# Optimization experiments

Measured on AMD Instinct MI355X. Metric: run time of the kernel, lower is better.

The kernel has to match this reference:

```python
import jax, jax.numpy as jnp
import numpy as np

B, L, E, H = 4, 4096, 1024, 16
HD = E // H
I = 4096  # intermediate_size = 4*E
RMS_EPS = 1e-6
ATTN_EPS = 1e-6
GATE_INIT = 0.1  # 0.1 + 0.05*layer_idx, layer_idx=0


def rmsnorm(x, w, eps=RMS_EPS):
    xf = x.astype(jnp.float32)
    var = jnp.mean(xf * xf, axis=-1, keepdims=True)
    return w * (xf * jax.lax.rsqrt(var + eps)).astype(x.dtype)


def rotate_half(x):
    d = x.shape[-1] // 2
    return jnp.concatenate([-x[..., d:], x[..., :d]], axis=-1)


def setup_inputs() -> dict:
    key = jax.random.key(0)
    ks = jax.random.split(key, 16)
    h = jax.random.normal(ks[0], (B, L, E), jnp.float32)
    c = jax.random.normal(ks[1], (B, E), jnp.float32)
    # standard RoPE tables, shape (L, HD)
    pos = jnp.arange(L, dtype=jnp.float32)
    inv = 1.0 / (10000.0 ** (jnp.arange(0, HD, 2, dtype=jnp.float32) / HD))
    fr = pos[:, None] * inv[None, :]
    emb = jnp.concatenate([fr, fr], axis=-1)
    cos, sin = jnp.cos(emb), jnp.sin(emb)
    s = 0.02
    Wq = jax.random.normal(ks[2], (E, E), jnp.float32) * s
    Wk = jax.random.normal(ks[3], (E, E), jnp.float32) * s
    Wv = jax.random.normal(ks[4], (E, E), jnp.float32) * s
    Wo = jax.random.normal(ks[5], (E, E), jnp.float32) * s
    Wg = jax.random.normal(ks[6], (I, E), jnp.float32) * s
    Wu = jax.random.normal(ks[7], (I, E), jnp.float32) * s
    Wd = jax.random.normal(ks[8], (E, I), jnp.float32) * s
    w_norm1 = jnp.ones((E,), jnp.float32)
    w_norm2 = jnp.ones((E,), jnp.float32)
    Wada = jax.random.normal(ks[9], (6 * E, E), jnp.float32) * 0.01
    bada = np.zeros((6 * E,), np.float32)
    bada[2 * E:3 * E] = GATE_INIT  # gate_msa
    bada[5 * E:6 * E] = GATE_INIT  # gate_mlp
    bada = jnp.asarray(bada)
    return {"h": h, "c": c, "cos": cos, "sin": sin, "Wq": Wq, "Wk": Wk,
            "Wv": Wv, "Wo": Wo, "Wg": Wg, "Wu": Wu, "Wd": Wd,
            "w_norm1": w_norm1, "w_norm2": w_norm2, "Wada": Wada, "bada": bada}


def reference(h, c, cos, sin, Wq, Wk, Wv, Wo, Wg, Wu, Wd, w_norm1, w_norm2, Wada, bada):
    # adaLN modulation: (B, 6E) -> six (B,1,E) chunks
    mod = c @ Wada.T + bada
    sh1, sc1, g1, sh2, sc2, g2 = [m[:, None, :] for m in jnp.split(mod, 6, axis=-1)]

    # --- attention branch ---
    x = rmsnorm(h, w_norm1) * (1.0 + sc1) + sh1  # modulate
    q = jax.nn.silu(x @ Wq.T).reshape(B, L, H, HD).transpose(0, 2, 1, 3)  # (B,H,L,hd)
    k = jax.nn.silu(x @ Wk.T).reshape(B, L, H, HD).transpose(0, 2, 1, 3)
    v = (x @ Wv.T).reshape(B, L, H, HD).transpose(0, 2, 1, 3)
    cs = cos[None, None]  # (1,1,L,hd)
    sn = sin[None, None]
    q = q * cs + rotate_half(q) * sn
    k = k * cs + rotate_half(k) * sn
    # cosFormer sin/cos feature map; m = max(src,tgt) = L
    idx = (np.pi / 2) * jnp.arange(1, L + 1, dtype=jnp.float32) / L  # (L,)
    sw = jnp.sin(idx)[None, None, :, None]
    cw = jnp.cos(idx)[None, None, :, None]
    q_ = jnp.concatenate([q * sw, q * cw], axis=-1)  # (B,H,L,2hd)
    k_ = jnp.concatenate([k * sw, k * cw], axis=-1)
    # non-causal linear attention: K^T V first (O(L))
    kv = jnp.einsum('bhld,bhlm->bhdm', k_, v)             # (B,H,2hd,hd)
    z = 1.0 / jnp.maximum(jnp.einsum('bhld,bhd->bhl', q_, k_.sum(axis=2)), ATTN_EPS)
    attn = jnp.einsum('bhld,bhdm,bhl->bhlm', q_, kv, z)   # (B,H,L,hd)
    attn = attn.transpose(0, 2, 1, 3).reshape(B, L, E) @ Wo.T
    h = h + g1 * attn  # bias_dropout_add_scale, eval mode

    # --- MLP branch ---
    x = rmsnorm(h, w_norm2) * (1.0 + sc2) + sh2
    mlp = (jax.nn.silu(x @ Wg.T) * (x @ Wu.T)) @ Wd.T
    return h + g2 * mlp
```

## Files before the change

kernel.cpp:

```cpp
#include <hip/hip_runtime.h>
#include <hip/hip_bf16.h>

#define BB 4
#define LL 4096
#define EE 1024
#define HH 16
#define II 4096
#define MM (BB*LL)

using f32x4 = __attribute__((ext_vector_type(4))) float;
using s16x8 = __attribute__((ext_vector_type(8))) short;
using u32x4 = __attribute__((ext_vector_type(4))) unsigned int;

__device__ __forceinline__ unsigned short f2bf(float f) {
  union { float f; unsigned u; } x; x.f = f;
  unsigned r = x.u + 0x7fffu + ((x.u >> 16) & 1u);
  return (unsigned short)(r >> 16);
}
__device__ __forceinline__ float bf2f(unsigned short s) {
  union { unsigned u; float f; } x; x.u = ((unsigned)s) << 16;
  return x.f;
}
__device__ __forceinline__ unsigned packbf(float lo, float hi) {
  return ((unsigned)f2bf(hi) << 16) | (unsigned)f2bf(lo);
}
__device__ __forceinline__ float silu_f(float x) { return x / (1.0f + expf(-x)); }

__global__ __launch_bounds__(256) void k_mod(const float* __restrict__ c,
    const float* __restrict__ Wada, const float* __restrict__ bada,
    float* __restrict__ mod) {
  __shared__ float cs[EE];
  int b = blockIdx.y;
  int n = blockIdx.x * 256 + threadIdx.x;
  for (int i = threadIdx.x; i < EE; i += 256) cs[i] = c[b*EE + i];
  __syncthreads();
  const float4* wp = (const float4*)(Wada + (size_t)n * EE);
  float acc = 0.f;
  for (int k = 0; k < EE/4; k++) {
    float4 t = wp[k];
    acc += t.x*cs[4*k] + t.y*cs[4*k+1] + t.z*cs[4*k+2] + t.w*cs[4*k+3];
  }
  mod[(size_t)b*6*EE + n] = acc + bada[n];
}

__global__ __launch_bounds__(256) void k_coef(const float* __restrict__ mod,
    const float* __restrict__ w1, const float* __restrict__ w2,
    float* __restrict__ cf1, float* __restrict__ cf2) {
  int k = blockIdx.x * 256 + threadIdx.x;
  int b = blockIdx.y;
  const float* mb = mod + (size_t)b*6*EE;
  cf1[(size_t)b*2048 + k]        = w1[k] * (1.0f + mb[EE + k]);
  cf1[(size_t)b*2048 + 1024 + k] = mb[k];
  cf2[(size_t)b*2048 + k]        = w2[k] * (1.0f + mb[4*EE + k]);
  cf2[(size_t)b*2048 + 1024 + k] = mb[3*EE + k];
}

__global__ __launch_bounds__(256) void k_rsig(const float* __restrict__ in,
    float* __restrict__ rsig) {
  int row = blockIdx.x;
  int t = threadIdx.x;
  float4 v = ((const float4*)(in + (size_t)row * EE))[t];
  float ss = v.x*v.x + v.y*v.y + v.z*v.z + v.w*v.w;
  #pragma unroll
  for (int o = 32; o > 0; o >>= 1) ss += __shfl_down(ss, o, 64);
  __shared__ float red[4];
  if ((t & 63) == 0) red[t >> 6] = ss;
  __syncthreads();
  float tot = red[0] + red[1] + red[2] + red[3];
  if (t == 0) rsig[row] = 1.0f / sqrtf(tot * (1.0f/1024.0f) + 1e-6f);
}

__global__ __launch_bounds__(256) void k_f2b(const float* __restrict__ s,
    unsigned short* __restrict__ d, int n4) {
  int i = blockIdx.x * 256 + threadIdx.x;
  if (i >= n4) return;
  float4 v = ((const float4*)s)[i];
  ushort4 u; u.x = f2bf(v.x); u.y = f2bf(v.y); u.z = f2bf(v.z); u.w = f2bf(v.w);
  ((ushort4*)d)[i] = u;
}

__global__ __launch_bounds__(256) void k_sgemm_qk(
    const float* __restrict__ Ah, const float* __restrict__ W,
    const float* __restrict__ rsig, const float* __restrict__ cf,
    const float* __restrict__ cosT, const float* __restrict__ sinT,
    float* __restrict__ outq) {
  __shared__ float As[8][128];
  __shared__ float Bs[8][128];
  __shared__ float c1s[1024];
  __shared__ float c0s[1024];
  int t = threadIdx.x;
  int tx = t & 15, ty = t >> 4;
  int bm = blockIdx.x, bn = blockIdx.y;
  int srow = t >> 1, sk = (t & 1) * 4;
  int bidx = bm >> 5;
  for (int i = t; i < 1024; i += 256) {
    c1s[i] = cf[(size_t)bidx*2048 + i];
    c0s[i] = cf[(size_t)bidx*2048 + 1024 + i];
  }
  int arow = bm*128 + srow;
  float rsA = rsig[arow];
  const float* ap = Ah + (size_t)arow*EE + sk;
  const float* bp = W + (size_t)(bn*128 + srow)*EE + sk;
  float acc[8][8];
  #pragma unroll
  for (int i = 0; i < 8; i++)
    #pragma unroll
    for (int j = 0; j < 8; j++) acc[i][j] = 0.f;
  float4 pa = *(const float4*)ap;
  float4 pb = *(const float4*)bp;
  int c0 = (tx < 8) ? tx*4 : 64 + (tx - 8)*4;
  __syncthreads();
  for (int k0 = 0; k0 < EE; k0 += 8) {
    int kb = k0 + sk;
    As[sk+0][srow] = fmaf(pa.x*rsA, c1s[kb+0], c0s[kb+0]);
    As[sk+1][srow] = fmaf(pa.y*rsA, c1s[kb+1], c0s[kb+1]);
    As[sk+2][srow] = fmaf(pa.z*rsA, c1s[kb+2], c0s[kb+2]);
    As[sk+3][srow] = fmaf(pa.w*rsA, c1s[kb+3], c0s[kb+3]);
    Bs[sk+0][srow] = pb.x; Bs[sk+1][srow] = pb.y; Bs[sk+2][srow] = pb.z; Bs[sk+3][srow] = pb.w;
    __syncthreads();
    if (k0 + 8 < EE) {
      pa = *(const float4*)(ap + k0 + 8);
      pb = *(const float4*)(bp + k0 + 8);
    }
    #pragma unroll
    for (int k = 0; k < 8; k++) {
      float4 a0 = *(const float4*)&As[k][ty*8];
      float4 a1 = *(const float4*)&As[k][ty*8+4];
      float4 b0 = *(const float4*)&Bs[k][c0];
      float4 b1 = *(const float4*)&Bs[k][c0+32];
      float av[8] = {a0.x,a0.y,a0.z,a0.w,a1.x,a1.y,a1.z,a1.w};
      float bv[8] = {b0.x,b0.y,b0.z,b0.w,b1.x,b1.y,b1.z,b1.w};
      #pragma unroll
      for (int i = 0; i < 8; i++)
        #pragma unroll
        for (int j = 0; j < 8; j++)
          acc[i][j] = fmaf(av[i], bv[j], acc[i][j]);
    }
    __syncthreads();
  }
  int head = bn*2 + (tx >= 8 ? 1 : 0);
  int d0 = (tx < 8) ? tx*4 : (tx - 8)*4;
  #pragma unroll
  for (int i = 0; i < 8; i++) {
    int m = bm*128 + ty*8 + i;
    int b = m >> 12, l = m & 4095;
    const float* cp = cosT + (size_t)l*64;
    const float* sp = sinT + (size_t)l*64;
    float4 cl  = *(const float4*)(cp + d0);
    float4 slv = *(const float4*)(sp + d0);
    float4 chv = *(const float4*)(cp + d0 + 32);
    float4 shv = *(const float4*)(sp + d0 + 32);
    float sA0 = silu_f(acc[i][0]), sA1 = silu_f(acc[i][1]), sA2 = silu_f(acc[i][2]), sA3 = silu_f(acc[i][3]);
    float sB0 = silu_f(acc[i][4]), sB1 = silu_f(acc[i][5]), sB2 = silu_f(acc[i][6]), sB3 = silu_f(acc[i][7]);
    float q00 = sA0*cl.x - sB0*slv.x;
    float q01 = sA1*cl.y - sB1*slv.y;
    float q02 = sA2*cl.z - sB2*slv.z;
    float q03 = sA3*cl.w - sB3*slv.w;
    float q10 = sB0*chv.x + sA0*shv.x;
    float q11 = sB1*chv.y + sA1*shv.y;
    float q12 = sB2*chv.z + sA2*shv.z;
    float q13 = sB3*chv.w + sA3*shv.w;
    float* op = outq + ((size_t)(b*HH + head)*LL + l)*64;
    *(float4*)(op + d0)      = make_float4(q00, q01, q02, q03);
    *(float4*)(op + d0 + 32) = make_float4(q10, q11, q12, q13);
  }
}

template<int EPI, int KD, int AMODE>
__global__ __launch_bounds__(256) void k_gemm_bt(
    const float* __restrict__ Af, const unsigned short* __restrict__ Ab,
    const unsigned short* __restrict__ Bw,
    const float* __restrict__ rsig, const float* __restrict__ cf,
    const float* __restrict__ res, const float* __restrict__ mod,
    unsigned short* __restrict__ outb, float* __restrict__ outf) {
  __shared__ unsigned short As[128][40];
  __shared__ unsigned short Bs[128][40];
  __shared__ float c1s[1024];
  __shared__ float c0s[1024];
  int t = threadIdx.x;
  int bm = blockIdx.x, bn = blockIdx.y;
  int w = t >> 6, lane = t & 63;
  int wm = (w >> 1) * 64, wn = (w & 1) * 64;
  f32x4 acc[4][4];
  #pragma unroll
  for (int i = 0; i < 4; i++)
    #pragma unroll
    for (int j = 0; j < 4; j++) acc[i][j] = (f32x4){0.f, 0.f, 0.f, 0.f};
  int srow = t >> 1, koff = (t & 1) * 16;
  int arow = bm*128 + srow;
  const unsigned short* bp = Bw + (size_t)(bn*128 + srow)*KD + koff;
  u32x4 pb0 = *(const u32x4*)bp;
  u32x4 pb1 = *(const u32x4*)(bp + 8);
  float rsA = 0.f;
  const float* apf = nullptr;
  const unsigned short* apb = nullptr;
  float4 ha0, ha1, ha2, ha3;
  u32x4 pa0, pa1;
  if constexpr (AMODE == 1) {
    int bidx = bm >> 5;
    for (int i = t; i < 1024; i += 256) {
      c1s[i] = cf[(size_t)bidx*2048 + i];
      c0s[i] = cf[(size_t)bidx*2048 + 1024 + i];
    }
    rsA = rsig[arow];
    apf = Af + (size_t)arow*KD + koff;
    ha0 = *(const float4*)apf;
    ha1 = *(const float4*)(apf + 4);
    ha2 = *(const float4*)(apf + 8);
    ha3 = *(const float4*)(apf + 12);
    __syncthreads();
  } else {
    apb = Ab + (size_t)arow*KD + koff;
    pa0 = *(const u32x4*)apb;
    pa1 = *(const u32x4*)(apb + 8);
  }
  int r16 = lane & 15, kg = lane >> 4;
  for (int k0 = 0; k0 < KD; k0 += 32) {
    if constexpr (AMODE == 1) {
      int kb = k0 + koff;
      float x0  = fmaf(ha0.x*rsA, c1s[kb+0],  c0s[kb+0]);
      float x1  = fmaf(ha0.y*rsA, c1s[kb+1],  c0s[kb+1]);
      float x2  = fmaf(ha0.z*rsA, c1s[kb+2],  c0s[kb+2]);
      float x3  = fmaf(ha0.w*rsA, c1s[kb+3],  c0s[kb+3]);
      float x4  = fmaf(ha1.x*rsA, c1s[kb+4],  c0s[kb+4]);
      float x5  = fmaf(ha1.y*rsA, c1s[kb+5],  c0s[kb+5]);
      float x6  = fmaf(ha1.z*rsA, c1s[kb+6],  c0s[kb+6]);
      float x7  = fmaf(ha1.w*rsA, c1s[kb+7],  c0s[kb+7]);
      float x8  = fmaf(ha2.x*rsA, c1s[kb+8],  c0s[kb+8]);
      float x9  = fmaf(ha2.y*rsA, c1s[kb+9],  c0s[kb+9]);
      float x10 = fmaf(ha2.z*rsA, c1s[kb+10], c0s[kb+10]);
      float x11 = fmaf(ha2.w*rsA, c1s[kb+11], c0s[kb+11]);
      float x12 = fmaf(ha3.x*rsA, c1s[kb+12], c0s[kb+12]);
      float x13 = fmaf(ha3.y*rsA, c1s[kb+13], c0s[kb+13]);
      float x14 = fmaf(ha3.z*rsA, c1s[kb+14], c0s[kb+14]);
      float x15 = fmaf(ha3.w*rsA, c1s[kb+15], c0s[kb+15]);
      u32x4 ua, ub;
      ua[0] = packbf(x0, x1);  ua[1] = packbf(x2, x3);
      ua[2] = packbf(x4, x5);  ua[3] = packbf(x6, x7);
      ub[0] = packbf(x8, x9);  ub[1] = packbf(x10, x11);
      ub[2] = packbf(x12, x13); ub[3] = packbf(x14, x15);
      *(u32x4*)&As[srow][koff]   = ua;
      *(u32x4*)&As[srow][koff+8] = ub;
    } else {
      *(u32x4*)&As[srow][koff]   = pa0;
      *(u32x4*)&As[srow][koff+8] = pa1;
    }
    *(u32x4*)&Bs[srow][koff]   = pb0;
    *(u32x4*)&Bs[srow][koff+8] = pb1;
    __syncthreads();
    if (k0 + 32 < KD) {
      if constexpr (AMODE == 1) {
        ha0 = *(const float4*)(apf + k0 + 32);
        ha1 = *(const float4*)(apf + k0 + 36);
        ha2 = *(const float4*)(apf + k0 + 40);
        ha3 = *(const float4*)(apf + k0 + 44);
      } else {
        pa0 = *(const u32x4*)(apb + k0 + 32);
        pa1 = *(const u32x4*)(apb + k0 + 40);
      }
      pb0 = *(const u32x4*)(bp + k0 + 32);
      pb1 = *(const u32x4*)(bp + k0 + 40);
    }
    s16x8 af[4], bfr[4];
    #pragma unroll
    for (int i = 0; i < 4; i++) af[i]  = *(const s16x8*)&As[wm + i*16 + r16][kg*8];
    #pragma unroll
    for (int j = 0; j < 4; j++) bfr[j] = *(const s16x8*)&Bs[wn + j*16 + r16][kg*8];
    #pragma unroll
    for (int i = 0; i < 4; i++)
      #pragma unroll
      for (int j = 0; j < 4; j++)
        acc[i][j] = __builtin_amdgcn_mfma_f32_16x16x32_bf16(af[i], bfr[j], acc[i][j], 0, 0, 0);
    __syncthreads();
  }
  #pragma unroll
  for (int i = 0; i < 4; i++) {
    #pragma unroll
    for (int j = 0; j < 4; j++) {
      int nn = bn*128 + wn + j*16 + r16;
      #pragma unroll
      for (int r = 0; r < 4; r++) {
        int mm = bm*128 + wm + i*16 + kg*4 + r;
        float v = acc[i][j][r];
        if constexpr (EPI == 0) {
          int b = mm >> 12, l = mm & 4095, hh = nn >> 6, dd = nn & 63;
          outb[(((size_t)(b*HH + hh))*LL + l)*64 + dd] = f2bf(v);
        } else if constexpr (EPI == 1) {
          int b = mm >> 12;
          size_t o = (size_t)mm*EE + nn;
          outf[o] = res[o] + mod[(size_t)b*6*EE + 2*EE + nn] * v;
        } else if constexpr (EPI == 2) {
          outb[(size_t)mm*II + nn] = f2bf(silu_f(v));
        } else if constexpr (EPI == 3) {
          size_t o = (size_t)mm*II + nn;
          outb[o] = f2bf(bf2f(outb[o]) * v);
        } else {
          int b = mm >> 12;
          size_t o = (size_t)mm*EE + nn;
          outf[o] = res[o] + mod[(size_t)b*6*EE + 5*EE + nn] * v;
        }
      }
    }
  }
}

__global__ __launch_bounds__(256) void k_kvpart(const float* __restrict__ kr,
    const unsigned short* __restrict__ vtb, float* __restrict__ kvp) {
  int bi = blockIdx.x;
  int bh = bi >> 3, ch = bi & 7;
  const float* kp = kr + ((size_t)bh*LL + ch*512)*64;
  const unsigned short* vp = vtb + ((size_t)bh*LL + ch*512)*64;
  __shared__ float k8[8][64];
  __shared__ float v8[8][64];
  __shared__ float sw8[8], cw8[8];
  int t = threadIdx.x;
  int d = t >> 2, mq = (t & 3) * 16;
  float accS[16], accC[16];
  #pragma unroll
  for (int q = 0; q < 16; q++) { accS[q] = 0.f; accC[q] = 0.f; }
  float ksS = 0.f, ksC = 0.f;
  for (int l0 = 0; l0 < 512; l0 += 8) {
    __syncthreads();
    #pragma unroll
    for (int rep = 0; rep < 2; rep++) {
      int idx = rep*256 + t;
      k8[idx>>6][idx&63] = kp[(size_t)(l0 + (idx>>6))*64 + (idx&63)];
      v8[idx>>6][idx&63] = bf2f(vp[(size_t)(l0 + (idx>>6))*64 + (idx&63)]);
    }
    if (t < 8) {
      int gl = ch*512 + l0 + t;
      float idxv = 1.5707964f * (float)(gl + 1) * (1.0f/4096.0f);
      sw8[t] = sinf(idxv);
      cw8[t] = cosf(idxv);
    }
    __syncthreads();
    #pragma unroll
    for (int l = 0; l < 8; l++) {
      float kd = k8[l][d];
      float s = kd * sw8[l];
      float c = kd * cw8[l];
      ksS += s; ksC += c;
      const float4* vv = (const float4*)&v8[l][mq];
      #pragma unroll
      for (int q = 0; q < 4; q++) {
        float4 x = vv[q];
        accS[4*q+0] = fmaf(s, x.x, accS[4*q+0]);
        accS[4*q+1] = fmaf(s, x.y, accS[4*q+1]);
        accS[4*q+2] = fmaf(s, x.z, accS[4*q+2]);
        accS[4*q+3] = fmaf(s, x.w, accS[4*q+3]);
        accC[4*q+0] = fmaf(c, x.x, accC[4*q+0]);
        accC[4*q+1] = fmaf(c, x.y, accC[4*q+1]);
        accC[4*q+2] = fmaf(c, x.z, accC[4*q+2]);
        accC[4*q+3] = fmaf(c, x.w, accC[4*q+3]);
      }
    }
  }
  float* op = kvp + (size_t)bi * 8320;
  #pragma unroll
  for (int q = 0; q < 16; q++) {
    op[d*64 + mq + q]        = accS[q];
    op[4096 + d*64 + mq + q] = accC[q];
  }
  if (mq == 0) { op[8192 + d] = ksS; op[8256 + d] = ksC; }
}

__global__ __launch_bounds__(256) void k_kvred(const float* __restrict__ kvp,
    float* __restrict__ kvb) {
  int bh = blockIdx.x;
  for (int i = threadIdx.x; i < 8320; i += 256) {
    float s = 0.f;
    #pragma unroll
    for (int c = 0; c < 8; c++) s += kvp[((size_t)bh*8 + c)*8320 + i];
    kvb[(size_t)bh*8320 + i] = s;
  }
}

__global__ __launch_bounds__(256) void k_z(const float* __restrict__ qr,
    const float* __restrict__ kvb, float* __restrict__ zb) {
  int bh = blockIdx.x >> 6, lc = blockIdx.x & 63;
  __shared__ float ksS_s[64], ksC_s[64];
  int t = threadIdx.x;
  if (t < 64) ksS_s[t] = kvb[(size_t)bh*8320 + 8192 + t];
  else if (t < 128) ksC_s[t-64] = kvb[(size_t)bh*8320 + 8256 + (t-64)];
  __syncthreads();
  int l = lc*64 + (t >> 2), part = t & 3;
  const float4* qp = (const float4*)(qr + ((size_t)bh*LL + l)*64 + part*16);
  float A = 0.f, Bv = 0.f;
  #pragma unroll
  for (int q = 0; q < 4; q++) {
    float4 x = qp[q];
    int kb = part*16 + 4*q;
    A  += x.x*ksS_s[kb] + x.y*ksS_s[kb+1] + x.z*ksS_s[kb+2] + x.w*ksS_s[kb+3];
    Bv += x.x*ksC_s[kb] + x.y*ksC_s[kb+1] + x.z*ksC_s[kb+2] + x.w*ksC_s[kb+3];
  }
  A  += __shfl_xor(A, 1, 64);  A  += __shfl_xor(A, 2, 64);
  Bv += __shfl_xor(Bv, 1, 64); Bv += __shfl_xor(Bv, 2, 64);
  if (part == 0) {
    float idxv = 1.5707964f * (float)(l + 1) * (1.0f/4096.0f);
    float denom = sinf(idxv)*A + cosf(idxv)*Bv;
    zb[(size_t)bh*LL + l] = 1.0f / fmaxf(denom, 1e-6f);
  }
}

__global__ __launch_bounds__(256) void k_attn(const float* __restrict__ qr,
    const float* __restrict__ kvb, const float* __restrict__ zb,
    unsigned short* __restrict__ attnb) {
  int bh = blockIdx.x >> 4, lc = blockIdx.x & 15;
  int t = threadIdx.x, w = t >> 6, lane = t & 63;
  const float* kvp_ = kvb + (size_t)bh*8320;
  float kvS[64], kvC[64];
  #pragma unroll
  for (int d = 0; d < 64; d++) kvS[d] = kvp_[d*64 + lane];
  #pragma unroll
  for (int d = 0; d < 64; d++) kvC[d] = kvp_[4096 + d*64 + lane];
  int b = bh >> 4, hh = bh & 15;
  int lbase = lc*256 + w*64;
  for (int li = 0; li < 64; li++) {
    int l = lbase + li;
    const float* qp = qr + ((size_t)bh*LL + l)*64;
    float qv = qp[lane];
    float z = zb[(size_t)bh*LL + l];
    float a0 = 0.f, a1 = 0.f, a2 = 0.f, a3 = 0.f;
    float b0 = 0.f, b1 = 0.f, b2 = 0.f, b3 = 0.f;
    #pragma unroll
    for (int d = 0; d < 64; d += 4) {
      float q0 = __uint_as_float(__builtin_amdgcn_readlane(__float_as_uint(qv), d+0));
      float q1 = __uint_as_float(__builtin_amdgcn_readlane(__float_as_uint(qv), d+1));
      float q2 = __uint_as_float(__builtin_amdgcn_readlane(__float_as_uint(qv), d+2));
      float q3 = __uint_as_float(__builtin_amdgcn_readlane(__float_as_uint(qv), d+3));
      a0 = fmaf(q0, kvS[d+0], a0);
      a1 = fmaf(q1, kvS[d+1], a1);
      a2 = fmaf(q2, kvS[d+2], a2);
      a3 = fmaf(q3, kvS[d+3], a3);
      b0 = fmaf(q0, kvC[d+0], b0);
      b1 = fmaf(q1, kvC[d+1], b1);
      b2 = fmaf(q2, kvC[d+2], b2);
      b3 = fmaf(q3, kvC[d+3], b3);
    }
    float A = (a0 + a1) + (a2 + a3);
    float Bv = (b0 + b1) + (b2 + b3);
    float idxv = 1.5707964f * (float)(l + 1) * (1.0f/4096.0f);
    float num = sinf(idxv)*A + cosf(idxv)*Bv;
    attnb[(((size_t)b*LL + l)*HH + hh)*64 + lane] = f2bf(num * z);
  }
}

extern "C" void kernel_launch(void* const* d_in, const int* in_sizes, int n_in,
                              void* d_out, int out_size, void* d_ws, size_t ws_size,
                              hipStream_t stream) {
  const float* h    = (const float*)d_in[0];
  const float* c    = (const float*)d_in[1];
  const float* cosT = (const float*)d_in[2];
  const float* sinT = (const float*)d_in[3];
  const float* Wq   = (const float*)d_in[4];
  const float* Wk   = (const float*)d_in[5];
  const float* Wv   = (const float*)d_in[6];
  const float* Wo   = (const float*)d_in[7];
  const float* Wg   = (const float*)d_in[8];
  const float* Wu   = (const float*)d_in[9];
  const float* Wd   = (const float*)d_in[10];
  const float* w1   = (const float*)d_in[11];
  const float* w2   = (const float*)d_in[12];
  const float* Wada = (const float*)d_in[13];
  const float* bada = (const float*)d_in[14];
  float* out = (float*)d_out;

  constexpr size_t BIG_SZ   = (size_t)MM * II * 2;
  constexpr size_t WS_NEEDED = BIG_SZ + 131072 + 32768*2 + 65536*2
      + 1048576 + 2129920 + 2097152*2 + 8388608*3;
  if (ws_size < WS_NEEDED) return;

  char* p = (char*)d_ws;
  char* big = p;                               p += BIG_SZ;
  float* mod = (float*)p;                      p += 131072;
  float* cf1 = (float*)p;                      p += 32768;
  float* cf2 = (float*)p;                      p += 32768;
  float* rsig1 = (float*)p;                    p += 65536;
  float* rsig2 = (float*)p;                    p += 65536;
  float* zb  = (float*)p;                      p += 1048576;
  float* kvb = (float*)p;                      p += 2129920;
  unsigned short* Wvb = (unsigned short*)p;    p += 2097152;
  unsigned short* Wob = (unsigned short*)p;    p += 2097152;
  unsigned short* Wgb = (unsigned short*)p;    p += 8388608;
  unsigned short* Wub = (unsigned short*)p;    p += 8388608;
  unsigned short* Wdb = (unsigned short*)p;    p += 8388608;
  float* kr            = (float*)big;
  unsigned short* vtb  = (unsigned short*)(big + 67108864);
  float* kvp           = (float*)(big + 100663296);
  float* qr            = (float*)big;
  unsigned short* attnb= (unsigned short*)(big + 67108864);
  unsigned short* Gb   = (unsigned short*)big;

  k_mod<<<dim3(24, BB), 256, 0, stream>>>(c, Wada, bada, mod);
  k_coef<<<dim3(4, BB), 256, 0, stream>>>(mod, w1, w2, cf1, cf2);
  k_rsig<<<MM, 256, 0, stream>>>(h, rsig1);
  k_f2b<<<1024, 256, 0, stream>>>(Wv, Wvb, EE*EE/4);
  k_f2b<<<1024, 256, 0, stream>>>(Wo, Wob, EE*EE/4);
  k_f2b<<<4096, 256, 0, stream>>>(Wg, Wgb, II*EE/4);
  k_f2b<<<4096, 256, 0, stream>>>(Wu, Wub, II*EE/4);
  k_f2b<<<4096, 256, 0, stream>>>(Wd, Wdb, EE*II/4);

  k_sgemm_qk<<<dim3(128, 8), 256, 0, stream>>>(h, Wk, rsig1, cf1, cosT, sinT, kr);
  k_gemm_bt<0, EE, 1><<<dim3(128, 8), 256, 0, stream>>>(
      h, nullptr, Wvb, rsig1, cf1, nullptr, nullptr, vtb, nullptr);
  k_kvpart<<<BB*HH*8, 256, 0, stream>>>(kr, vtb, kvp);
  k_kvred<<<BB*HH, 256, 0, stream>>>(kvp, kvb);

  k_sgemm_qk<<<dim3(128, 8), 256, 0, stream>>>(h, Wq, rsig1, cf1, cosT, sinT, qr);
  k_z<<<BB*HH*(LL/64), 256, 0, stream>>>(qr, kvb, zb);
  k_attn<<<BB*HH*(LL/256), 256, 0, stream>>>(qr, kvb, zb, attnb);

  k_gemm_bt<1, EE, 0><<<dim3(128, 8), 256, 0, stream>>>(
      nullptr, attnb, Wob, nullptr, nullptr, h, mod, nullptr, out);

  k_rsig<<<MM, 256, 0, stream>>>(out, rsig2);
  k_gemm_bt<2, EE, 1><<<dim3(128, 32), 256, 0, stream>>>(
      out, nullptr, Wgb, rsig2, cf2, nullptr, nullptr, Gb, nullptr);
  k_gemm_bt<3, EE, 1><<<dim3(128, 32), 256, 0, stream>>>(
      out, nullptr, Wub, rsig2, cf2, nullptr, nullptr, Gb, nullptr);
  k_gemm_bt<4, II, 0><<<dim3(128, 8), 256, 0, stream>>>(
      nullptr, Gb, Wdb, nullptr, nullptr, out, mod, nullptr, out);
}
```

Measured before the change: 2.148 ms.

## Use split-bf16 MFMA for Q projection, async LDS loads, and near-zero denominator fixup

Several changes land together. The normalized activations are precomputed once into hi/lo bf16 pairs. The fp32 SIMT Q GEMM is replaced by a three-term split-bf16 MFMA GEMM, which emulates near-fp32 accuracy on matrix cores. All bf16 GEMMs now stage tiles with global_load_lds direct-to-LDS copies and an XOR swizzle instead of register staging. To guard accuracy, rows whose attention denominator is near zero are collected with an atomic list and recomputed in double precision. This adds a pre-pass kernel, extra MFMAs, and a fixup kernel whose cost depends on how many rows are flagged.

```diff
diff --git a/kernel.cpp b/kernel.cpp
--- a/kernel.cpp
+++ b/kernel.cpp
@@ -25,6 +25,12 @@
   return ((unsigned)f2bf(hi) << 16) | (unsigned)f2bf(lo);
 }
 __device__ __forceinline__ float silu_f(float x) { return x / (1.0f + expf(-x)); }
+
+__device__ __forceinline__ void gll16(const void* g, void* l) {
+  __builtin_amdgcn_global_load_lds(
+      (const __attribute__((address_space(1))) unsigned int*)g,
+      (__attribute__((address_space(3))) unsigned int*)l, 16, 0, 0);
+}
 
 __global__ __launch_bounds__(256) void k_mod(const float* __restrict__ c,
     const float* __restrict__ Wada, const float* __restrict__ bada,
@@ -79,7 +85,31 @@
   ((ushort4*)d)[i] = u;
 }
 
-__global__ __launch_bounds__(256) void k_sgemm_qk(
+__global__ __launch_bounds__(256) void k_split1(const float* __restrict__ h,
+    const float* __restrict__ rsig, const float* __restrict__ cf,
+    unsigned short* __restrict__ xh, unsigned short* __restrict__ xl) {
+  int row = blockIdx.x;
+  int t = threadIdx.x;
+  int b = row >> 12;
+  float rs = rsig[row];
+  const float* cfb = cf + (size_t)b*2048;
+  float4 v  = ((const float4*)(h + (size_t)row*EE))[t];
+  float4 c1 = ((const float4*)cfb)[t];
+  float4 c0 = ((const float4*)(cfb + 1024))[t];
+  float x0 = fmaf(v.x*rs, c1.x, c0.x);
+  float x1 = fmaf(v.y*rs, c1.y, c0.y);
+  float x2 = fmaf(v.z*rs, c1.z, c0.z);
+  float x3 = fmaf(v.w*rs, c1.w, c0.w);
+  ushort4 uh, ul;
+  uh.x = f2bf(x0); ul.x = f2bf(x0 - bf2f(uh.x));
+  uh.y = f2bf(x1); ul.y = f2bf(x1 - bf2f(uh.y));
+  uh.z = f2bf(x2); ul.z = f2bf(x2 - bf2f(uh.z));
+  uh.w = f2bf(x3); ul.w = f2bf(x3 - bf2f(uh.w));
+  ((ushort4*)(xh + (size_t)row*EE))[t] = uh;
+  ((ushort4*)(xl + (size_t)row*EE))[t] = ul;
+}
+
+__global__ __launch_bounds__(256) void k_sgemmK(
     const float* __restrict__ Ah, const float* __restrict__ W,
     const float* __restrict__ rsig, const float* __restrict__ cf,
     const float* __restrict__ cosT, const float* __restrict__ sinT,
@@ -129,7 +159,7 @@
       float4 b0 = *(const float4*)&Bs[k][c0];
       float4 b1 = *(const float4*)&Bs[k][c0+32];
       float av[8] = {a0.x,a0.y,a0.z,a0.w,a1.x,a1.y,a1.z,a1.w};
-      float bv[8] = {b0.x,b0.y,b0.z,b0.w,b1.x,b1.y,b1.z,b1.w};
+      float bv[8]  = {b0.x,b0.y,b0.z,b0.w,b1.x,b1.y,b1.z,b1.w};
       #pragma unroll
       for (int i = 0; i < 8; i++)
         #pragma unroll
@@ -166,57 +196,162 @@
   }
 }
 
+__global__ __launch_bounds__(256) void k_qk(
+    const unsigned short* __restrict__ xh, const unsigned short* __restrict__ xl,
+    const float* __restrict__ W,
+    const float* __restrict__ cosT, const float* __restrict__ sinT,
+    float* __restrict__ outq) {
+  __shared__ unsigned short Ah[128*32];
+  __shared__ unsigned short Al[128*32];
+  __shared__ unsigned short Bh[64*40];
+  __shared__ unsigned short Bl[64*40];
+  int t = threadIdx.x, w = t >> 6, lane = t & 63;
+  int bm = blockIdx.x, bn = blockIdx.y;
+  int wm = (w & 1) * 64;
+  int wn = (w >> 1) * 16;
+  int r16 = lane & 15, kg = lane >> 4;
+  int rin = lane >> 2, slot = lane & 3;
+  int ar0 = w*32 + rin, ar1 = ar0 + 16;
+  const unsigned short* ahg0 = xh + (size_t)(bm*128 + ar0)*EE + (size_t)((((ar0>>1)&3) ^ slot) * 8);
+  const unsigned short* ahg1 = xh + (size_t)(bm*128 + ar1)*EE + (size_t)((((ar1>>1)&3) ^ slot) * 8);
+  const unsigned short* alg0 = xl + (size_t)(bm*128 + ar0)*EE + (size_t)((((ar0>>1)&3) ^ slot) * 8);
+  const unsigned short* alg1 = xl + (size_t)(bm*128 + ar1)*EE + (size_t)((((ar1>>1)&3) ^ slot) * 8);
+  unsigned short* ahl0 = &Ah[(w*32 + 0) * 32];
+  unsigned short* ahl1 = &Ah[(w*32 + 16) * 32];
+  unsigned short* all0 = &Al[(w*32 + 0) * 32];
+  unsigned short* all1 = &Al[(w*32 + 16) * 32];
+  int srow = t >> 2, koff = (t & 3) * 8;
+  const float* bp = W + (size_t)(bn*64 + srow)*EE + koff;
+  float4 pb0 = *(const float4*)(bp + 0);
+  float4 pb1 = *(const float4*)(bp + 4);
+  f32x4 acc[4][2];
+  #pragma unroll
+  for (int i = 0; i < 4; i++) { acc[i][0] = (f32x4){0,0,0,0}; acc[i][1] = (f32x4){0,0,0,0}; }
+
+  for (int k0 = 0; k0 < EE; k0 += 32) {
+    gll16(ahg0 + k0, ahl0);
+    gll16(ahg1 + k0, ahl1);
+    gll16(alg0 + k0, all0);
+    gll16(alg1 + k0, all1);
+    {
+      unsigned short h0 = f2bf(pb0.x), h1 = f2bf(pb0.y), h2 = f2bf(pb0.z), h3 = f2bf(pb0.w);
+      unsigned short h4 = f2bf(pb1.x), h5 = f2bf(pb1.y), h6 = f2bf(pb1.z), h7 = f2bf(pb1.w);
+      unsigned short l0 = f2bf(pb0.x - bf2f(h0)), l1 = f2bf(pb0.y - bf2f(h1));
+      unsigned short l2 = f2bf(pb0.z - bf2f(h2)), l3 = f2bf(pb0.w - bf2f(h3));
+      unsigned short l4 = f2bf(pb1.x - bf2f(h4)), l5 = f2bf(pb1.y - bf2f(h5));
+      unsigned short l6 = f2bf(pb1.z - bf2f(h6)), l7 = f2bf(pb1.w - bf2f(h7));
+      u32x4 uh, ul;
+      uh[0] = ((unsigned)h1<<16)|h0; uh[1] = ((unsigned)h3<<16)|h2;
+      uh[2] = ((unsigned)h5<<16)|h4; uh[3] = ((unsigned)h7<<16)|h6;
+      ul[0] = ((unsigned)l1<<16)|l0; ul[1] = ((unsigned)l3<<16)|l2;
+      ul[2] = ((unsigned)l5<<16)|l4; ul[3] = ((unsigned)l7<<16)|l6;
+      *(u32x4*)&Bh[srow*40 + koff] = uh;
+      *(u32x4*)&Bl[srow*40 + koff] = ul;
+    }
+    __syncthreads();
+    if (k0 + 32 < EE) {
+      pb0 = *(const float4*)(bp + k0 + 32);
+      pb1 = *(const float4*)(bp + k0 + 36);
+    }
+    int brow0 = wn + r16, brow1 = wn + 32 + r16;
+    s16x8 bh0 = *(const s16x8*)&Bh[brow0*40 + kg*8];
+    s16x8 bl0 = *(const s16x8*)&Bl[brow0*40 + kg*8];
+    s16x8 bh1 = *(const s16x8*)&Bh[brow1*40 + kg*8];
+    s16x8 bl1 = *(const s16x8*)&Bl[brow1*40 + kg*8];
+    #pragma unroll
+    for (int i = 0; i < 4; i++) {
+      int row = wm + i*16 + r16;
+      int sw = ((((row>>1)&3) ^ kg) << 3);
+      s16x8 ah = *(const s16x8*)&Ah[row*32 + sw];
+      s16x8 al = *(const s16x8*)&Al[row*32 + sw];
+      acc[i][0] = __builtin_amdgcn_mfma_f32_16x16x32_bf16(ah, bh0, acc[i][0], 0, 0, 0);
+      acc[i][0] = __builtin_amdgcn_mfma_f32_16x16x32_bf16(ah, bl0, acc[i][0], 0, 0, 0);
+      acc[i][0] = __builtin_amdgcn_mfma_f32_16x16x32_bf16(al, bh0, acc[i][0], 0, 0, 0);
+      acc[i][1] = __builtin_amdgcn_mfma_f32_16x16x32_bf16(ah, bh1, acc[i][1], 0, 0, 0);
+      acc[i][1] = __builtin_amdgcn_mfma_f32_16x16x32_bf16(ah, bl1, acc[i][1], 0, 0, 0);
+      acc[i][1] = __builtin_amdgcn_mfma_f32_16x16x32_bf16(al, bh1, acc[i][1], 0, 0, 0);
+    }
+    __syncthreads();
+  }
+  int d = wn + r16;
+  #pragma unroll
+  for (int i = 0; i < 4; i++) {
+    #pragma unroll
+    for (int r = 0; r < 4; r++) {
+      int mm = bm*128 + wm + i*16 + kg*4 + r;
+      int b = mm >> 12, l = mm & 4095;
+      const float* cp = cosT + (size_t)l*64;
+      const float* sp = sinT + (size_t)l*64;
+      float sl = silu_f(acc[i][0][r]);
+      float sh = silu_f(acc[i][1][r]);
+      float qlo = sl*cp[d]      - sh*sp[d];
+      float qhi = sh*cp[d + 32] + sl*sp[d + 32];
+      float* op = outq + (((size_t)(b*HH + bn))*LL + l)*64;
+      op[d]      = qlo;
+      op[d + 32] = qhi;
+    }
+  }
+}
+
 template<int EPI, int KD, int AMODE>
-__global__ __launch_bounds__(256) void k_gemm_bt(
+__global__ __launch_bounds__(256) void k_gemm2(
     const float* __restrict__ Af, const unsigned short* __restrict__ Ab,
     const unsigned short* __restrict__ Bw,
     const float* __restrict__ rsig, const float* __restrict__ cf,
     const float* __restrict__ res, const float* __restrict__ mod,
     unsigned short* __restrict__ outb, float* __restrict__ outf) {
-  __shared__ unsigned short As[128][40];
-  __shared__ unsigned short Bs[128][40];
-  __shared__ float c1s[1024];
-  __shared__ float c0s[1024];
-  int t = threadIdx.x;
+  constexpr int APAD = (AMODE == 1) ? 40 : 32;
+  __shared__ unsigned short As[128 * APAD];
+  __shared__ unsigned short Bs[128 * 32];
+  __shared__ float c1s[(AMODE == 1) ? 1024 : 1];
+  __shared__ float c0s[(AMODE == 1) ? 1024 : 1];
+  int t = threadIdx.x, w = t >> 6, lane = t & 63;
   int bm = blockIdx.x, bn = blockIdx.y;
-  int w = t >> 6, lane = t & 63;
   int wm = (w >> 1) * 64, wn = (w & 1) * 64;
-  f32x4 acc[4][4];
-  #pragma unroll
-  for (int i = 0; i < 4; i++)
-    #pragma unroll
-    for (int j = 0; j < 4; j++) acc[i][j] = (f32x4){0.f, 0.f, 0.f, 0.f};
+  int rin = lane >> 2, slot = lane & 3;
+  int brow0 = w*32 + rin, brow1 = brow0 + 16;
+  const unsigned short* bg0 = Bw + (size_t)(bn*128 + brow0)*KD + (size_t)((((brow0>>1)&3) ^ slot) * 8);
+  const unsigned short* bg1 = Bw + (size_t)(bn*128 + brow1)*KD + (size_t)((((brow1>>1)&3) ^ slot) * 8);
+  unsigned short* bl0 = &Bs[(w*32 + 0) * 32];
+  unsigned short* bl1 = &Bs[(w*32 + 16) * 32];
+  const unsigned short* ag0 = nullptr; const unsigned short* ag1 = nullptr;
+  unsigned short* al0 = nullptr; unsigned short* al1 = nullptr;
+  const float* apf = nullptr;
+  float rsA = 0.f;
   int srow = t >> 1, koff = (t & 1) * 16;
-  int arow = bm*128 + srow;
-  const unsigned short* bp = Bw + (size_t)(bn*128 + srow)*KD + koff;
-  u32x4 pb0 = *(const u32x4*)bp;
-  u32x4 pb1 = *(const u32x4*)(bp + 8);
-  float rsA = 0.f;
-  const float* apf = nullptr;
-  const unsigned short* apb = nullptr;
   float4 ha0, ha1, ha2, ha3;
-  u32x4 pa0, pa1;
   if constexpr (AMODE == 1) {
     int bidx = bm >> 5;
     for (int i = t; i < 1024; i += 256) {
       c1s[i] = cf[(size_t)bidx*2048 + i];
       c0s[i] = cf[(size_t)bidx*2048 + 1024 + i];
     }
-    rsA = rsig[arow];
-    apf = Af + (size_t)arow*KD + koff;
-    ha0 = *(const float4*)apf;
+    rsA = rsig[bm*128 + srow];
+    apf = Af + (size_t)(bm*128 + srow)*KD + koff;
+    ha0 = *(const float4*)(apf + 0);
     ha1 = *(const float4*)(apf + 4);
     ha2 = *(const float4*)(apf + 8);
     ha3 = *(const float4*)(apf + 12);
     __syncthreads();
   } else {
-    apb = Ab + (size_t)arow*KD + koff;
-    pa0 = *(const u32x4*)apb;
-    pa1 = *(const u32x4*)(apb + 8);
-  }
+    ag0 = Ab + (size_t)(bm*128 + brow0)*KD + (size_t)((((brow0>>1)&3) ^ slot) * 8);
+    ag1 = Ab + (size_t)(bm*128 + brow1)*KD + (size_t)((((brow1>>1)&3) ^ slot) * 8);
+    al0 = &As[(w*32 + 0) * 32];
+    al1 = &As[(w*32 + 16) * 32];
+  }
+  f32x4 acc[4][4];
+  #pragma unroll
+  for (int i = 0; i < 4; i++)
+    #pragma unroll
+    for (int j = 0; j < 4; j++) acc[i][j] = (f32x4){0.f, 0.f, 0.f, 0.f};
   int r16 = lane & 15, kg = lane >> 4;
   for (int k0 = 0; k0 < KD; k0 += 32) {
-    if constexpr (AMODE == 1) {
+    gll16(bg0 + k0, bl0);
+    gll16(bg1 + k0, bl1);
+    if constexpr (AMODE == 0) {
+      gll16(ag0 + k0, al0);
+      gll16(ag1 + k0, al1);
+    } else {
       int kb = k0 + koff;
       float x0  = fmaf(ha0.x*rsA, c1s[kb+0],  c0s[kb+0]);
       float x1  = fmaf(ha0.y*rsA, c1s[kb+1],  c0s[kb+1]);
@@ -235,37 +370,36 @@
       float x14 = fmaf(ha3.z*rsA, c1s[kb+14], c0s[kb+14]);
       float x15 = fmaf(ha3.w*rsA, c1s[kb+15], c0s[kb+15]);
       u32x4 ua, ub;
-      ua[0] = packbf(x0, x1);  ua[1] = packbf(x2, x3);
-      ua[2] = packbf(x4, x5);  ua[3] = packbf(x6, x7);
-      ub[0] = packbf(x8, x9);  ub[1] = packbf(x10, x11);
+      ua[0] = packbf(x0, x1);   ua[1] = packbf(x2, x3);
+      ua[2] = packbf(x4, x5);   ua[3] = packbf(x6, x7);
+      ub[0] = packbf(x8, x9);   ub[1] = packbf(x10, x11);
       ub[2] = packbf(x12, x13); ub[3] = packbf(x14, x15);
-      *(u32x4*)&As[srow][koff]   = ua;
-      *(u32x4*)&As[srow][koff+8] = ub;
-    } else {
-      *(u32x4*)&As[srow][koff]   = pa0;
-      *(u32x4*)&As[srow][koff+8] = pa1;
-    }
-    *(u32x4*)&Bs[srow][koff]   = pb0;
-    *(u32x4*)&Bs[srow][koff+8] = pb1;
-    __syncthreads();
-    if (k0 + 32 < KD) {
-      if constexpr (AMODE == 1) {
+      *(u32x4*)&As[srow*APAD + koff]     = ua;
+      *(u32x4*)&As[srow*APAD + koff + 8] = ub;
+    }
+    __syncthreads();
+    if constexpr (AMODE == 1) {
+      if (k0 + 32 < KD) {
         ha0 = *(const float4*)(apf + k0 + 32);
         ha1 = *(const float4*)(apf + k0 + 36);
         ha2 = *(const float4*)(apf + k0 + 40);
         ha3 = *(const float4*)(apf + k0 + 44);
-      } else {
-        pa0 = *(const u32x4*)(apb + k0 + 32);
-        pa1 = *(const u32x4*)(apb + k0 + 40);
       }
-      pb0 = *(const u32x4*)(bp + k0 + 32);
-      pb1 = *(const u32x4*)(bp + k0 + 40);
     }
     s16x8 af[4], bfr[4];
     #pragma unroll
-    for (int i = 0; i < 4; i++) af[i]  = *(const s16x8*)&As[wm + i*16 + r16][kg*8];
-    #pragma unroll
-    for (int j = 0; j < 4; j++) bfr[j] = *(const s16x8*)&Bs[wn + j*16 + r16][kg*8];
+    for (int i = 0; i < 4; i++) {
+      int row = wm + i*16 + r16;
+      if constexpr (AMODE == 0)
+        af[i] = *(const s16x8*)&As[row*32 + ((((row>>1)&3) ^ kg) << 3)];
+      else
+        af[i] = *(const s16x8*)&As[row*APAD + (kg << 3)];
+    }
+    #pragma unroll
+    for (int j = 0; j < 4; j++) {
+      int row = wn + j*16 + r16;
+      bfr[j] = *(const s16x8*)&Bs[row*32 + ((((row>>1)&3) ^ kg) << 3)];
+    }
     #pragma unroll
     for (int i = 0; i < 4; i++)
       #pragma unroll
@@ -375,8 +509,11 @@
   }
 }
 
+__global__ void k_zero(int* __restrict__ cnt) { if (threadIdx.x == 0) *cnt = 0; }
+
 __global__ __launch_bounds__(256) void k_z(const float* __restrict__ qr,
-    const float* __restrict__ kvb, float* __restrict__ zb) {
+    const float* __restrict__ kvb, float* __restrict__ zb,
+    int* __restrict__ list, int* __restrict__ cnt) {
   int bh = blockIdx.x >> 6, lc = blockIdx.x & 63;
   __shared__ float ksS_s[64], ksC_s[64];
   int t = threadIdx.x;
@@ -398,7 +535,67 @@
   if (part == 0) {
     float idxv = 1.5707964f * (float)(l + 1) * (1.0f/4096.0f);
     float denom = sinf(idxv)*A + cosf(idxv)*Bv;
-    zb[(size_t)bh*LL + l] = 1.0f / fmaxf(denom, 1e-6f);
+    int gid = bh*LL + l;
+    zb[gid] = 1.0f / fmaxf(denom, 1e-6f);
+    if (fabsf(denom) < 0.05f) {
+      int idx = atomicAdd(cnt, 1);
+      list[idx] = gid;
+    }
+  }
+}
+
+__global__ __launch_bounds__(256) void k_zfix(const float* __restrict__ h,
+    const float* __restrict__ rsig, const float* __restrict__ cf,
+    const float* __restrict__ Wq,
+    const float* __restrict__ cosT, const float* __restrict__ sinT,
+    const float* __restrict__ kvb, const int* __restrict__ list,
+    const int* __restrict__ cnt, float* __restrict__ zb) {
+  __shared__ float xs[1024];
+  __shared__ double qd[64];
+  __shared__ double sq[64];
+  int n = *cnt;
+  int t = threadIdx.x;
+  for (int i = blockIdx.x; i < n; i += gridDim.x) {
+    int gid = list[i];
+    int bh = gid >> 12, l = gid & 4095;
+    int b = bh >> 4, hh = bh & 15;
+    int row = b*4096 + l;
+    float rs = rsig[row];
+    const float* cfb = cf + (size_t)b*2048;
+    for (int k = t; k < 1024; k += 256)
+      xs[k] = fmaf(h[(size_t)row*1024 + k]*rs, cfb[k], cfb[1024 + k]);
+    __syncthreads();
+    int j = t >> 2, s = t & 3;
+    const float* wrow = Wq + (size_t)(hh*64 + j)*1024 + s*256;
+    double acc = 0.0;
+    for (int k = 0; k < 256; k++)
+      acc += (double)wrow[k] * (double)xs[s*256 + k];
+    acc += __shfl_xor(acc, 1, 64);
+    acc += __shfl_xor(acc, 2, 64);
+    if (s == 0) qd[j] = acc;
+    __syncthreads();
+    if (t < 64) {
+      double qv = qd[t];
+      sq[t] = qv / (1.0 + exp(-qv));
+    }
+    __syncthreads();
+    if (t == 0) {
+      const float* cp = cosT + (size_t)l*64;
+      const float* sp = sinT + (size_t)l*64;
+      const float* ksS = kvb + (size_t)bh*8320 + 8192;
+      const float* ksC = kvb + (size_t)bh*8320 + 8256;
+      double dS = 0.0, dC = 0.0;
+      for (int d = 0; d < 64; d++) {
+        double rot = (d < 32) ? -sq[d + 32] : sq[d - 32];
+        double qe = sq[d]*(double)cp[d] + rot*(double)sp[d];
+        dS += qe * (double)ksS[d];
+        dC += qe * (double)ksC[d];
+      }
+      double idxv = 1.5707963267948966 * (double)(l + 1) / 4096.0;
+      float denom = (float)(sin(idxv)*dS + cos(idxv)*dC);
+      zb[gid] = 1.0f / fmaxf(denom, 1e-6f);
+    }
+    __syncthreads();
   }
 }
 
@@ -484,12 +681,16 @@
   unsigned short* Wgb = (unsigned short*)p;    p += 8388608;
   unsigned short* Wub = (unsigned short*)p;    p += 8388608;
   unsigned short* Wdb = (unsigned short*)p;    p += 8388608;
-  float* kr            = (float*)big;
+  unsigned short* xh   = (unsigned short*)big;
+  unsigned short* xl   = (unsigned short*)(big + 33554432);
   unsigned short* vtb  = (unsigned short*)(big + 67108864);
   float* kvp           = (float*)(big + 100663296);
-  float* qr            = (float*)big;
-  unsigned short* attnb= (unsigned short*)(big + 67108864);
+  float* qr            = (float*)(big + 67108864);
+  int* zf_cnt          = (int*)big;
+  int* zf_list         = (int*)(big + 256);
+  unsigned short* attnb= (unsigned short*)big;
   unsigned short* Gb   = (unsigned short*)big;
+  float* kr            = (float*)d_out;
 
   k_mod<<<dim3(24, BB), 256, 0, stream>>>(c, Wada, bada, mod);
   k_coef<<<dim3(4, BB), 256, 0, stream>>>(mod, w1, w2, cf1, cf2);
@@ -499,25 +700,29 @@
   k_f2b<<<4096, 256, 0, stream>>>(Wg, Wgb, II*EE/4);
   k_f2b<<<4096, 256, 0, stream>>>(Wu, Wub, II*EE/4);
   k_f2b<<<4096, 256, 0, stream>>>(Wd, Wdb, EE*II/4);
-
-  k_sgemm_qk<<<dim3(128, 8), 256, 0, stream>>>(h, Wk, rsig1, cf1, cosT, sinT, kr);
-  k_gemm_bt<0, EE, 1><<<dim3(128, 8), 256, 0, stream>>>(
-      h, nullptr, Wvb, rsig1, cf1, nullptr, nullptr, vtb, nullptr);
+  k_split1<<<MM, 256, 0, stream>>>(h, rsig1, cf1, xh, xl);
+
+  k_sgemmK<<<dim3(128, 8), 256, 0, stream>>>(h, Wk, rsig1, cf1, cosT, sinT, kr);
+  k_gemm2<0, EE, 0><<<dim3(128, 8), 256, 0, stream>>>(
+      nullptr, xh, Wvb, nullptr, nullptr, nullptr, nullptr, vtb, nullptr);
   k_kvpart<<<BB*HH*8, 256, 0, stream>>>(kr, vtb, kvp);
   k_kvred<<<BB*HH, 256, 0, stream>>>(kvp, kvb);
 
-  k_sgemm_qk<<<dim3(128, 8), 256, 0, stream>>>(h, Wq, rsig1, cf1, cosT, sinT, qr);
-  k_z<<<BB*HH*(LL/64), 256, 0, stream>>>(qr, kvb, zb);
+  k_qk<<<dim3(128, 16), 256, 0, stream>>>(xh, xl, Wq, cosT, sinT, qr);
+  k_zero<<<1, 64, 0, stream>>>(zf_cnt);
+  k_z<<<BB*HH*(LL/64), 256, 0, stream>>>(qr, kvb, zb, zf_list, zf_cnt);
+  k_zfix<<<120, 256, 0, stream>>>(h, rsig1, cf1, Wq, cosT, sinT, kvb,
+                                  zf_list, zf_cnt, zb);
   k_attn<<<BB*HH*(LL/256), 256, 0, stream>>>(qr, kvb, zb, attnb);
 
-  k_gemm_bt<1, EE, 0><<<dim3(128, 8), 256, 0, stream>>>(
+  k_gemm2<1, EE, 0><<<dim3(128, 8), 256, 0, stream>>>(
       nullptr, attnb, Wob, nullptr, nullptr, h, mod, nullptr, out);
 
   k_rsig<<<MM, 256, 0, stream>>>(out, rsig2);
-  k_gemm_bt<2, EE, 1><<<dim3(128, 32), 256, 0, stream>>>(
+  k_gemm2<2, EE, 1><<<dim3(128, 32), 256, 0, stream>>>(
       out, nullptr, Wgb, rsig2, cf2, nullptr, nullptr, Gb, nullptr);
-  k_gemm_bt<3, EE, 1><<<dim3(128, 32), 256, 0, stream>>>(
+  k_gemm2<3, EE, 1><<<dim3(128, 32), 256, 0, stream>>>(
       out, nullptr, Wub, rsig2, cf2, nullptr, nullptr, Gb, nullptr);
-  k_gemm_bt<4, II, 0><<<dim3(128, 8), 256, 0, stream>>>(
+  k_gemm2<4, II, 0><<<dim3(128, 8), 256, 0, stream>>>(
       nullptr, Gb, Wdb, nullptr, nullptr, out, mod, nullptr, out);
 }
```

Result: faster. 1.854 ms (-13.7%).
